# Kernel tuning notes

Measured on AMD Instinct MI355X. Metric: run time of the kernel, lower is better.

## Reference

```python
import jax, jax.numpy as jnp
import numpy as np

B, S, C = 8, 1024, 1280   # B = 2*N (uncond|cond halves), S = 32*32 latent tokens
H, D = 20, 64             # heads, head_dim; H*D == C


def setup_inputs() -> dict:
    key = jax.random.key(0)
    ks = jax.random.split(key, 5)
    std = 1.0 / np.sqrt(C)
    return {
        "hidden_states": jax.random.normal(ks[0], (B, S, C), jnp.float32),
        "Wq": jax.random.normal(ks[1], (C, C), jnp.float32) * std,
        "Wk": jax.random.normal(ks[2], (C, C), jnp.float32) * std,
        "Wv": jax.random.normal(ks[3], (C, C), jnp.float32) * std,
        "Wo": jax.random.normal(ks[4], (C, C), jnp.float32) * std,
        "bo": jnp.zeros((C,), jnp.float32),
    }


def _inject(x, n):
    # replicate reference rows 0 (uncond) and n (cond) across each half
    unc = jnp.broadcast_to(x[0:1], (n,) + x.shape[1:])
    con = jnp.broadcast_to(x[n:n + 1], (n,) + x.shape[1:])
    return jnp.concatenate([unc, con], axis=0)


def reference(hidden_states, Wq, Wk, Wv, Wo, bo):
    b, s, c = hidden_states.shape
    n = b // 2
    q = hidden_states @ Wq
    k = hidden_states @ Wk
    v = hidden_states @ Wv
    # PnP injection (self-attention, share_enabled, n > 1, all injections on)
    q = _inject(q, n)
    k = _inject(k, n)
    v = _inject(v, n)
    # head split: [b, s, c] -> [b, h, s, d]
    q = q.reshape(b, s, H, D).transpose(0, 2, 1, 3)
    k = k.reshape(b, s, H, D).transpose(0, 2, 1, 3)
    v = v.reshape(b, s, H, D).transpose(0, 2, 1, 3)
    scale = 1.0 / np.sqrt(D)
    scores = jnp.einsum("bhqd,bhkd->bhqk", q, k) * scale
    probs = jax.nn.softmax(scores, axis=-1)
    out = jnp.einsum("bhqk,bhkd->bhqd", probs, v)
    out = out.transpose(0, 2, 1, 3).reshape(b, s, c)
    return out @ Wo + bo
```

## Files before the change

### kernel.cpp

```cpp
#include <hip/hip_runtime.h>

#define S_LEN 1024
#define C_DIM 1280
#define NH 20
#define HD 64

typedef __attribute__((ext_vector_type(8))) short short8;
typedef __attribute__((ext_vector_type(4))) short short4v;
typedef __attribute__((ext_vector_type(4))) float float4v;

__device__ __forceinline__ float bf2f(unsigned short u) {
    union { unsigned u; float f; } v; v.u = ((unsigned)u) << 16; return v.f;
}
__device__ __forceinline__ unsigned short f2bf(float f) {
    union { float f; unsigned u; } v; v.f = f;
    unsigned u = v.u;
    return (unsigned short)((u + 0x7FFFu + ((u >> 16) & 1u)) >> 16);
}

__device__ __forceinline__ void load_lds16(const unsigned short* g, unsigned short* l) {
    __builtin_amdgcn_global_load_lds(
        (const __attribute__((address_space(1))) unsigned int*)g,
        (__attribute__((address_space(3))) unsigned int*)l, 16, 0, 0);
}

__global__ __launch_bounds__(256) void detect_kernel(
    const unsigned int* __restrict__ w, int* __restrict__ flag)
{
    __shared__ int cnt;
    if (threadIdx.x == 0) cnt = 0;
    __syncthreads();
    int local = 0;
    for (int i = threadIdx.x; i < 1024; i += 256) {
        unsigned e = (w[i] >> 7) & 0xFFu;
        if (e >= 100u && e <= 140u) local++;
    }
    atomicAdd(&cnt, local);
    __syncthreads();
    if (threadIdx.x == 0) *flag = (cnt < 512) ? 1 : 0;
}

__global__ __launch_bounds__(256) void convx_kernel(
    const void* __restrict__ hs, const int* __restrict__ flag,
    unsigned short* __restrict__ X)
{
    const size_t SC = (size_t)S_LEN * C_DIM;
    int g = blockIdx.y;
    size_t off = ((size_t)blockIdx.x * 256 + threadIdx.x) * 8;
    size_t src = (size_t)g * 4 * SC + off;
    short8 o;
    if (*flag) {
        const float* p = (const float*)hs + src;
        for (int j = 0; j < 8; j++) o[j] = (short)f2bf(p[j]);
    } else {
        o = *(const short8*)((const unsigned short*)hs + src);
    }
    *(short8*)(X + g * SC + off) = o;
}

__global__ __launch_bounds__(256) void convw_kernel(
    const void* __restrict__ Wq, const void* __restrict__ Wk,
    const void* __restrict__ Wv, const void* __restrict__ Wo,
    const int* __restrict__ flag, unsigned short* __restrict__ WT)
{
    __shared__ unsigned short tile[64 * 68];
    const void* W = (blockIdx.z == 0) ? Wq : (blockIdx.z == 1) ? Wk
                    : (blockIdx.z == 2) ? Wv : Wo;
    unsigned short* T = WT + (size_t)blockIdx.z * C_DIM * C_DIM;
    int fp32 = *flag;
    int c0 = blockIdx.x * 64, r0 = blockIdx.y * 64;
    int t = threadIdx.x;
    int r = t >> 3, cg = t & 7;
    for (int rep = 0; rep < 2; rep++) {
        int rr = r0 + r + rep * 32;
        if (fp32) {
            const float* p = (const float*)W + (size_t)rr * C_DIM + c0 + cg * 8;
            for (int j = 0; j < 8; j++)
                tile[(r + rep * 32) * 68 + cg * 8 + j] = f2bf(p[j]);
        } else {
            short8 v = *(const short8*)((const unsigned short*)W + (size_t)rr * C_DIM + c0 + cg * 8);
            for (int j = 0; j < 8; j++)
                tile[(r + rep * 32) * 68 + cg * 8 + j] = (unsigned short)v[j];
        }
    }
    __syncthreads();
    int c = t >> 3, rg = t & 7;
    for (int rep = 0; rep < 2; rep++) {
        short8 o;
        for (int j = 0; j < 8; j++)
            o[j] = (short)tile[(rg * 8 + j) * 68 + c + rep * 32];
        *(short8*)(T + (size_t)(c0 + c + rep * 32) * C_DIM + r0 + rg * 8) = o;
    }
}

__global__ __launch_bounds__(256) void gemm_qkv_kernel(
    const unsigned short* __restrict__ X,
    const unsigned short* __restrict__ WT,
    unsigned short* __restrict__ Qo, unsigned short* __restrict__ Ko,
    unsigned short* __restrict__ Vt)
{
    __shared__ __align__(16) unsigned short Al[2][64 * 64];
    __shared__ __align__(16) unsigned short Bl[2][128 * 64];
    int z = blockIdx.z;
    const unsigned short* Wt = WT + (size_t)z * C_DIM * C_DIM;
    int c0 = blockIdx.x * 128, r0 = blockIdx.y * 64;
    int t = threadIdx.x, wave = t >> 6, lane = t & 63;
    int quad = lane >> 4, mn = lane & 15;
    int srow = wave * 8 + (lane >> 3), slot = lane & 7;
    const unsigned short* xb = X + (size_t)r0 * C_DIM;
    const unsigned short* wb = Wt + (size_t)c0 * C_DIM;

    for (int p = 0; p < 2; p++) {
        int row = p * 32 + srow; int ck = slot ^ (row & 7);
        load_lds16(xb + (size_t)row * C_DIM + ck * 8, &Al[0][row * 64 + slot * 8]);
    }
    for (int p = 0; p < 4; p++) {
        int row = p * 32 + srow; int ck = slot ^ (row & 7);
        load_lds16(wb + (size_t)row * C_DIM + ck * 8, &Bl[0][row * 64 + slot * 8]);
    }
    asm volatile("s_waitcnt vmcnt(0)" ::: "memory");
    __builtin_amdgcn_s_barrier();

    float4v acc[4][2] = {};
    for (int kt = 0; kt < 20; kt++) {
        int cur = kt & 1, nxt = cur ^ 1;
        if (kt < 19) {
            int k0 = (kt + 1) * 64;
            for (int p = 0; p < 2; p++) {
                int row = p * 32 + srow; int ck = slot ^ (row & 7);
                load_lds16(xb + (size_t)row * C_DIM + k0 + ck * 8, &Al[nxt][row * 64 + slot * 8]);
            }
            for (int p = 0; p < 4; p++) {
                int row = p * 32 + srow; int ck = slot ^ (row & 7);
                load_lds16(wb + (size_t)row * C_DIM + k0 + ck * 8, &Bl[nxt][row * 64 + slot * 8]);
            }
        }
        for (int kc = 0; kc < 2; kc++) {
            short8 a[4], b[2];
            for (int mt = 0; mt < 4; mt++) {
                int row = mt * 16 + mn;
                a[mt] = *(const short8*)(&Al[cur][row * 64 + (((kc * 4 + quad) ^ (row & 7)) * 8)]);
            }
            for (int nt = 0; nt < 2; nt++) {
                int row = wave * 32 + nt * 16 + mn;
                b[nt] = *(const short8*)(&Bl[cur][row * 64 + (((kc * 4 + quad) ^ (row & 7)) * 8)]);
            }
            for (int mt = 0; mt < 4; mt++)
                for (int nt = 0; nt < 2; nt++)
                    acc[mt][nt] = __builtin_amdgcn_mfma_f32_16x16x32_bf16(a[mt], b[nt], acc[mt][nt], 0, 0, 0);
        }
        asm volatile("s_waitcnt vmcnt(0)" ::: "memory");
        __builtin_amdgcn_s_barrier();
    }

    if (z == 2) {
        int g = r0 >> 10;
        for (int mt = 0; mt < 4; mt++) {
            int row = r0 + mt * 16 + quad * 4;
            int s = row & 1023;
            for (int nt = 0; nt < 2; nt++) {
                int col = c0 + wave * 32 + nt * 16 + mn;
                short4v p;
                for (int i = 0; i < 4; i++) p[i] = (short)f2bf(acc[mt][nt][i]);
                *(short4v*)(Vt + ((size_t)g * C_DIM + col) * S_LEN + s) = p;
            }
        }
    } else {
        unsigned short* Out = (z == 0) ? Qo : Ko;
        for (int mt = 0; mt < 4; mt++) {
            int row = r0 + mt * 16 + quad * 4;
            for (int nt = 0; nt < 2; nt++) {
                int col = c0 + wave * 32 + nt * 16 + mn;
                for (int i = 0; i < 4; i++)
                    Out[(size_t)(row + i) * C_DIM + col] = f2bf(acc[mt][nt][i]);
            }
        }
    }
}

__global__ __launch_bounds__(256) void attn_kernel(
    const unsigned short* __restrict__ Q, const unsigned short* __restrict__ K,
    const unsigned short* __restrict__ VT, unsigned short* __restrict__ O)
{
    __shared__ __align__(16) unsigned short Kl[2][64 * 64];
    __shared__ __align__(16) unsigned short Vl[2][64 * 64];
    __shared__ unsigned short Pl[4 * 16 * 72];
    int qt = blockIdx.x, h = blockIdx.y, g = blockIdx.z;
    int t = threadIdx.x, wave = t >> 6, lane = t & 63;
    int quad = lane >> 4, n = lane & 15;
    const size_t SC = (size_t)S_LEN * C_DIM;
    const unsigned short* Qb = Q + (size_t)g * SC;
    const unsigned short* Kb = K + (size_t)g * SC + h * HD;
    const unsigned short* Vb = VT + (size_t)g * SC + (size_t)(h * HD) * S_LEN;
    unsigned short* Pw = &Pl[wave * 16 * 72];

    int srow = wave * 8 + (lane >> 3);
    int slot = lane & 7;

    short8 qa[2];
    int qrow = qt * 64 + wave * 16 + n;
    for (int kc = 0; kc < 2; kc++) {
        short8 v = *(const short8*)(Qb + (size_t)qrow * C_DIM + h * HD + kc * 32 + quad * 8);
        short8 w;
        for (int j = 0; j < 8; j++)
            w[j] = (short)f2bf(bf2f((unsigned short)v[j]) * 0.125f);
        qa[kc] = w;
    }

    for (int p = 0; p < 2; p++) {
        int row = p * 32 + srow;
        int ck = slot ^ (row & 7);
        load_lds16(Kb + (size_t)row * C_DIM + ck * 8, &Kl[0][row * 64 + slot * 8]);
        load_lds16(Vb + (size_t)row * S_LEN + ck * 8, &Vl[0][row * 64 + slot * 8]);
    }
    asm volatile("s_waitcnt vmcnt(0)" ::: "memory");
    __builtin_amdgcn_s_barrier();

    float4v oacc[4] = {};
    float lsum[4] = { 0.f, 0.f, 0.f, 0.f };

    for (int kt = 0; kt < 16; kt++) {
        int cur = kt & 1, nxt = cur ^ 1;
        if (kt < 15) {
            for (int p = 0; p < 2; p++) {
                int row = p * 32 + srow;
                int ck = slot ^ (row & 7);
                load_lds16(Kb + (size_t)((kt + 1) * 64 + row) * C_DIM + ck * 8,
                           &Kl[nxt][row * 64 + slot * 8]);
                load_lds16(Vb + (size_t)row * S_LEN + (kt + 1) * 64 + ck * 8,
                           &Vl[nxt][row * 64 + slot * 8]);
            }
        }
        const unsigned short* Kt = Kl[cur];
        const unsigned short* Vt = Vl[cur];

        float4v sacc[4] = {};
        for (int kc = 0; kc < 2; kc++)
            for (int nt = 0; nt < 4; nt++) {
                int row = nt * 16 + n;
                short8 kb = *(const short8*)(Kt + row * 64 + (((kc * 4 + quad) ^ (row & 7)) * 8));
                sacc[nt] = __builtin_amdgcn_mfma_f32_16x16x32_bf16(qa[kc], kb, sacc[nt], 0, 0, 0);
            }

        for (int nt = 0; nt < 4; nt++)
            for (int i = 0; i < 4; i++) {
                float p = __expf(sacc[nt][i]);
                lsum[i] += p;
                Pw[(quad * 4 + i) * 72 + nt * 16 + n] = f2bf(p);
            }
        asm volatile("s_waitcnt lgkmcnt(0)" ::: "memory");
        short8 pa0 = *(const short8*)(&Pw[n * 72 + quad * 8]);
        short8 pa1 = *(const short8*)(&Pw[n * 72 + 32 + quad * 8]);
        for (int kc = 0; kc < 2; kc++) {
            short8 pa = kc ? pa1 : pa0;
            for (int nt = 0; nt < 4; nt++) {
                int row = nt * 16 + n;
                short8 vb = *(const short8*)(Vt + row * 64 + (((kc * 4 + quad) ^ (row & 7)) * 8));
                oacc[nt] = __builtin_amdgcn_mfma_f32_16x16x32_bf16(pa, vb, oacc[nt], 0, 0, 0);
            }
        }
        asm volatile("s_waitcnt vmcnt(0)" ::: "memory");
        __builtin_amdgcn_s_barrier();
    }

    for (int i = 0; i < 4; i++)
        for (int d = 1; d < 16; d <<= 1)
            lsum[i] += __shfl_xor(lsum[i], d, 64);
    float inv[4];
    for (int i = 0; i < 4; i++) inv[i] = 1.0f / lsum[i];

    int row0 = qt * 64 + wave * 16 + quad * 4;
    for (int nt = 0; nt < 4; nt++)
        for (int i = 0; i < 4; i++)
            O[(size_t)g * SC + (size_t)(row0 + i) * C_DIM + h * HD + nt * 16 + n] =
                f2bf(oacc[nt][i] * inv[i]);
}

__global__ __launch_bounds__(256) void gemm_out_kernel(
    const unsigned short* __restrict__ X,
    const unsigned short* __restrict__ WoT,
    const void* __restrict__ bo,
    const int* __restrict__ flag,
    void* __restrict__ out)
{
    __shared__ __align__(16) unsigned short Al[2][64 * 64];
    __shared__ __align__(16) unsigned short Bl[2][64 * 64];
    int c0 = blockIdx.x * 64, r0 = blockIdx.y * 64;
    int t = threadIdx.x, wave = t >> 6, lane = t & 63;
    int wr = wave >> 1, wc = wave & 1, quad = lane >> 4, mn = lane & 15;
    int srow = wave * 8 + (lane >> 3), slot = lane & 7;
    const unsigned short* xb = X + (size_t)r0 * C_DIM;
    const unsigned short* wb = WoT + (size_t)c0 * C_DIM;
    int fp32 = *flag;

    for (int p = 0; p < 2; p++) {
        int row = p * 32 + srow; int ck = slot ^ (row & 7);
        load_lds16(xb + (size_t)row * C_DIM + ck * 8, &Al[0][row * 64 + slot * 8]);
        load_lds16(wb + (size_t)row * C_DIM + ck * 8, &Bl[0][row * 64 + slot * 8]);
    }
    asm volatile("s_waitcnt vmcnt(0)" ::: "memory");
    __builtin_amdgcn_s_barrier();

    float4v acc[2][2] = {};
    for (int kt = 0; kt < 20; kt++) {
        int cur = kt & 1, nxt = cur ^ 1;
        if (kt < 19) {
            int k0 = (kt + 1) * 64;
            for (int p = 0; p < 2; p++) {
                int row = p * 32 + srow; int ck = slot ^ (row & 7);
                load_lds16(xb + (size_t)row * C_DIM + k0 + ck * 8, &Al[nxt][row * 64 + slot * 8]);
                load_lds16(wb + (size_t)row * C_DIM + k0 + ck * 8, &Bl[nxt][row * 64 + slot * 8]);
            }
        }
        for (int kc = 0; kc < 2; kc++) {
            short8 a[2], b[2];
            for (int mt = 0; mt < 2; mt++) {
                int row = wr * 32 + mt * 16 + mn;
                a[mt] = *(const short8*)(&Al[cur][row * 64 + (((kc * 4 + quad) ^ (row & 7)) * 8)]);
            }
            for (int nt = 0; nt < 2; nt++) {
                int row = wc * 32 + nt * 16 + mn;
                b[nt] = *(const short8*)(&Bl[cur][row * 64 + (((kc * 4 + quad) ^ (row & 7)) * 8)]);
            }
            for (int mt = 0; mt < 2; mt++)
                for (int nt = 0; nt < 2; nt++)
                    acc[mt][nt] = __builtin_amdgcn_mfma_f32_16x16x32_bf16(a[mt], b[nt], acc[mt][nt], 0, 0, 0);
        }
        asm volatile("s_waitcnt vmcnt(0)" ::: "memory");
        __builtin_amdgcn_s_barrier();
    }

    for (int mt = 0; mt < 2; mt++) {
        int row = r0 + wr * 32 + mt * 16 + quad * 4;
        int g = row >> 10;
        for (int nt = 0; nt < 2; nt++) {
            int col = c0 + wc * 32 + nt * 16 + mn;
            float bb = fp32 ? ((const float*)bo)[col] : bf2f(((const unsigned short*)bo)[col]);
            for (int i = 0; i < 4; i++) {
                float v = acc[mt][nt][i] + bb;
                int s = (row + i) & 1023;
                if (fp32) {
                    float* o = (float*)out;
                    for (int rep = 0; rep < 4; rep++)
                        o[((size_t)(g * 4 + rep) * S_LEN + s) * C_DIM + col] = v;
                } else {
                    unsigned short* o = (unsigned short*)out;
                    unsigned short bv = f2bf(v);
                    for (int rep = 0; rep < 4; rep++)
                        o[((size_t)(g * 4 + rep) * S_LEN + s) * C_DIM + col] = bv;
                }
            }
        }
    }
}

extern "C" void kernel_launch(void* const* d_in, const int* in_sizes, int n_in,
                              void* d_out, int out_size, void* d_ws, size_t ws_size,
                              hipStream_t stream)
{
    const void* hs = d_in[0];
    const void* Wq = d_in[1];
    const void* Wk = d_in[2];
    const void* Wv = d_in[3];
    const void* Wo = d_in[4];
    const void* bo = d_in[5];

    const size_t CC  = (size_t)C_DIM * C_DIM;
    const size_t SC2 = (size_t)2 * S_LEN * C_DIM;

    int* flag = (int*)d_ws;
    unsigned short* base = (unsigned short*)((char*)d_ws + 256);
    unsigned short* WT = base;
    unsigned short* X  = WT + 4 * CC;
    unsigned short* Q  = X + SC2;
    unsigned short* K  = Q + SC2;
    unsigned short* VT = K + SC2;

    hipLaunchKernelGGL(detect_kernel, dim3(1), dim3(256), 0, stream,
                       (const unsigned int*)Wq, flag);
    hipLaunchKernelGGL(convx_kernel, dim3(640, 2), dim3(256), 0, stream,
                       hs, flag, X);
    hipLaunchKernelGGL(convw_kernel, dim3(20, 20, 4), dim3(256), 0, stream,
                       Wq, Wk, Wv, Wo, flag, WT);
    hipLaunchKernelGGL(gemm_qkv_kernel, dim3(10, 32, 3), dim3(256), 0, stream,
                       X, WT, Q, K, VT);
    hipLaunchKernelGGL(attn_kernel, dim3(16, NH, 2), dim3(256), 0, stream,
                       Q, K, VT, X );
    hipLaunchKernelGGL(gemm_out_kernel, dim3(20, 32), dim3(256), 0, stream,
                       X, WT + 3 * CC, bo, flag, d_out);
}
```

Baseline: 219.8 us.

## Switch GEMM and attention LDS staging to triple-buffered prefetch with partial vmcnt waits

All three kernels move from double-buffered to triple-buffered LDS tiles, prefetching two k-tiles ahead. Each iteration now waits only for the oldest outstanding loads (vmcnt(N)) and uses a single barrier at the top instead of draining all loads at the end. This keeps global-to-LDS loads in flight across iterations and removes one barrier per step. In exchange it uses 50% more LDS per block, which may lower occupancy, and correctness depends on the vmcnt counts matching the per-thread load count per stage.

```diff
diff --git a/kernel.cpp b/kernel.cpp
--- a/kernel.cpp
+++ b/kernel.cpp
@@ -99,8 +99,8 @@
     unsigned short* __restrict__ Qo, unsigned short* __restrict__ Ko,
     unsigned short* __restrict__ Vt)
 {
-    __shared__ __align__(16) unsigned short Al[2][64 * 64];
-    __shared__ __align__(16) unsigned short Bl[2][128 * 64];
+    __shared__ __align__(16) unsigned short Al[3][64 * 64];
+    __shared__ __align__(16) unsigned short Bl[3][128 * 64];
     int z = blockIdx.z;
     const unsigned short* Wt = WT + (size_t)z * C_DIM * C_DIM;
     int c0 = blockIdx.x * 128, r0 = blockIdx.y * 64;
@@ -110,30 +110,30 @@
     const unsigned short* xb = X + (size_t)r0 * C_DIM;
     const unsigned short* wb = Wt + (size_t)c0 * C_DIM;
 
-    for (int p = 0; p < 2; p++) {
-        int row = p * 32 + srow; int ck = slot ^ (row & 7);
-        load_lds16(xb + (size_t)row * C_DIM + ck * 8, &Al[0][row * 64 + slot * 8]);
-    }
-    for (int p = 0; p < 4; p++) {
-        int row = p * 32 + srow; int ck = slot ^ (row & 7);
-        load_lds16(wb + (size_t)row * C_DIM + ck * 8, &Bl[0][row * 64 + slot * 8]);
-    }
-    asm volatile("s_waitcnt vmcnt(0)" ::: "memory");
-    __builtin_amdgcn_s_barrier();
+    auto stage = [&](int ki, int buf) {
+        int k0 = ki * 64;
+        for (int p = 0; p < 2; p++) {
+            int row = p * 32 + srow; int ck = slot ^ (row & 7);
+            load_lds16(xb + (size_t)row * C_DIM + k0 + ck * 8, &Al[buf][row * 64 + slot * 8]);
+        }
+        for (int p = 0; p < 4; p++) {
+            int row = p * 32 + srow; int ck = slot ^ (row & 7);
+            load_lds16(wb + (size_t)row * C_DIM + k0 + ck * 8, &Bl[buf][row * 64 + slot * 8]);
+        }
+    };
+
+    stage(0, 0);
+    stage(1, 1);
 
     float4v acc[4][2] = {};
+    int cur = 0;
     for (int kt = 0; kt < 20; kt++) {
-        int cur = kt & 1, nxt = cur ^ 1;
-        if (kt < 19) {
-            int k0 = (kt + 1) * 64;
-            for (int p = 0; p < 2; p++) {
-                int row = p * 32 + srow; int ck = slot ^ (row & 7);
-                load_lds16(xb + (size_t)row * C_DIM + k0 + ck * 8, &Al[nxt][row * 64 + slot * 8]);
-            }
-            for (int p = 0; p < 4; p++) {
-                int row = p * 32 + srow; int ck = slot ^ (row & 7);
-                load_lds16(wb + (size_t)row * C_DIM + k0 + ck * 8, &Bl[nxt][row * 64 + slot * 8]);
-            }
+        if (kt < 19) asm volatile("s_waitcnt vmcnt(6)" ::: "memory");
+        else         asm volatile("s_waitcnt vmcnt(0)" ::: "memory");
+        __builtin_amdgcn_s_barrier();
+        if (kt + 2 < 20) {
+            int nb = cur + 2; if (nb >= 3) nb -= 3;
+            stage(kt + 2, nb);
         }
         for (int kc = 0; kc < 2; kc++) {
             short8 a[4], b[2];
@@ -149,8 +149,7 @@
                 for (int nt = 0; nt < 2; nt++)
                     acc[mt][nt] = __builtin_amdgcn_mfma_f32_16x16x32_bf16(a[mt], b[nt], acc[mt][nt], 0, 0, 0);
         }
-        asm volatile("s_waitcnt vmcnt(0)" ::: "memory");
-        __builtin_amdgcn_s_barrier();
+        cur++; if (cur == 3) cur = 0;
     }
 
     if (z == 2) {
@@ -182,8 +181,8 @@
     const unsigned short* __restrict__ Q, const unsigned short* __restrict__ K,
     const unsigned short* __restrict__ VT, unsigned short* __restrict__ O)
 {
-    __shared__ __align__(16) unsigned short Kl[2][64 * 64];
-    __shared__ __align__(16) unsigned short Vl[2][64 * 64];
+    __shared__ __align__(16) unsigned short Kl[3][64 * 64];
+    __shared__ __align__(16) unsigned short Vl[3][64 * 64];
     __shared__ unsigned short Pl[4 * 16 * 72];
     int qt = blockIdx.x, h = blockIdx.y, g = blockIdx.z;
     int t = threadIdx.x, wave = t >> 6, lane = t & 63;
@@ -207,29 +206,31 @@
         qa[kc] = w;
     }
 
-    for (int p = 0; p < 2; p++) {
-        int row = p * 32 + srow;
-        int ck = slot ^ (row & 7);
-        load_lds16(Kb + (size_t)row * C_DIM + ck * 8, &Kl[0][row * 64 + slot * 8]);
-        load_lds16(Vb + (size_t)row * S_LEN + ck * 8, &Vl[0][row * 64 + slot * 8]);
-    }
-    asm volatile("s_waitcnt vmcnt(0)" ::: "memory");
-    __builtin_amdgcn_s_barrier();
+    auto stage = [&](int ki, int buf) {
+        for (int p = 0; p < 2; p++) {
+            int row = p * 32 + srow;
+            int ck = slot ^ (row & 7);
+            load_lds16(Kb + (size_t)(ki * 64 + row) * C_DIM + ck * 8,
+                       &Kl[buf][row * 64 + slot * 8]);
+            load_lds16(Vb + (size_t)row * S_LEN + ki * 64 + ck * 8,
+                       &Vl[buf][row * 64 + slot * 8]);
+        }
+    };
+
+    stage(0, 0);
+    stage(1, 1);
 
     float4v oacc[4] = {};
     float lsum[4] = { 0.f, 0.f, 0.f, 0.f };
 
+    int cur = 0;
     for (int kt = 0; kt < 16; kt++) {
-        int cur = kt & 1, nxt = cur ^ 1;
-        if (kt < 15) {
-            for (int p = 0; p < 2; p++) {
-                int row = p * 32 + srow;
-                int ck = slot ^ (row & 7);
-                load_lds16(Kb + (size_t)((kt + 1) * 64 + row) * C_DIM + ck * 8,
-                           &Kl[nxt][row * 64 + slot * 8]);
-                load_lds16(Vb + (size_t)row * S_LEN + (kt + 1) * 64 + ck * 8,
-                           &Vl[nxt][row * 64 + slot * 8]);
-            }
+        if (kt < 15) asm volatile("s_waitcnt vmcnt(4)" ::: "memory");
+        else         asm volatile("s_waitcnt vmcnt(0)" ::: "memory");
+        __builtin_amdgcn_s_barrier();
+        if (kt + 2 < 16) {
+            int nb = cur + 2; if (nb >= 3) nb -= 3;
+            stage(kt + 2, nb);
         }
         const unsigned short* Kt = Kl[cur];
         const unsigned short* Vt = Vl[cur];
@@ -259,8 +260,7 @@
                 oacc[nt] = __builtin_amdgcn_mfma_f32_16x16x32_bf16(pa, vb, oacc[nt], 0, 0, 0);
             }
         }
-        asm volatile("s_waitcnt vmcnt(0)" ::: "memory");
-        __builtin_amdgcn_s_barrier();
+        cur++; if (cur == 3) cur = 0;
     }
 
     for (int i = 0; i < 4; i++)
@@ -283,8 +283,8 @@
     const int* __restrict__ flag,
     void* __restrict__ out)
 {
-    __shared__ __align__(16) unsigned short Al[2][64 * 64];
-    __shared__ __align__(16) unsigned short Bl[2][64 * 64];
+    __shared__ __align__(16) unsigned short Al[3][64 * 64];
+    __shared__ __align__(16) unsigned short Bl[3][64 * 64];
     int c0 = blockIdx.x * 64, r0 = blockIdx.y * 64;
     int t = threadIdx.x, wave = t >> 6, lane = t & 63;
     int wr = wave >> 1, wc = wave & 1, quad = lane >> 4, mn = lane & 15;
@@ -293,24 +293,27 @@
     const unsigned short* wb = WoT + (size_t)c0 * C_DIM;
     int fp32 = *flag;
 
-    for (int p = 0; p < 2; p++) {
-        int row = p * 32 + srow; int ck = slot ^ (row & 7);
-        load_lds16(xb + (size_t)row * C_DIM + ck * 8, &Al[0][row * 64 + slot * 8]);
-        load_lds16(wb + (size_t)row * C_DIM + ck * 8, &Bl[0][row * 64 + slot * 8]);
-    }
-    asm volatile("s_waitcnt vmcnt(0)" ::: "memory");
-    __builtin_amdgcn_s_barrier();
+    auto stage = [&](int ki, int buf) {
+        int k0 = ki * 64;
+        for (int p = 0; p < 2; p++) {
+            int row = p * 32 + srow; int ck = slot ^ (row & 7);
+            load_lds16(xb + (size_t)row * C_DIM + k0 + ck * 8, &Al[buf][row * 64 + slot * 8]);
+            load_lds16(wb + (size_t)row * C_DIM + k0 + ck * 8, &Bl[buf][row * 64 + slot * 8]);
+        }
+    };
+
+    stage(0, 0);
+    stage(1, 1);
 
     float4v acc[2][2] = {};
+    int cur = 0;
     for (int kt = 0; kt < 20; kt++) {
-        int cur = kt & 1, nxt = cur ^ 1;
-        if (kt < 19) {
-            int k0 = (kt + 1) * 64;
-            for (int p = 0; p < 2; p++) {
-                int row = p * 32 + srow; int ck = slot ^ (row & 7);
-                load_lds16(xb + (size_t)row * C_DIM + k0 + ck * 8, &Al[nxt][row * 64 + slot * 8]);
-                load_lds16(wb + (size_t)row * C_DIM + k0 + ck * 8, &Bl[nxt][row * 64 + slot * 8]);
-            }
+        if (kt < 19) asm volatile("s_waitcnt vmcnt(4)" ::: "memory");
+        else         asm volatile("s_waitcnt vmcnt(0)" ::: "memory");
+        __builtin_amdgcn_s_barrier();
+        if (kt + 2 < 20) {
+            int nb = cur + 2; if (nb >= 3) nb -= 3;
+            stage(kt + 2, nb);
         }
         for (int kc = 0; kc < 2; kc++) {
             short8 a[2], b[2];
@@ -326,8 +329,7 @@
                 for (int nt = 0; nt < 2; nt++)
                     acc[mt][nt] = __builtin_amdgcn_mfma_f32_16x16x32_bf16(a[mt], b[nt], acc[mt][nt], 0, 0, 0);
         }
-        asm volatile("s_waitcnt vmcnt(0)" ::: "memory");
-        __builtin_amdgcn_s_barrier();
+        cur++; if (cur == 3) cur = 0;
     }
 
     for (int mt = 0; mt < 2; mt++) {
```

Result: slower. 224.4 us (+2.1%).
